# Kernel tuning notes

Hardware: AMD Instinct MI355X
Metric: run time of the kernel (lower is better)

Reference implementation:

```python
import jax, jax.numpy as jnp
import numpy as np

K_HOPS = 2


def setup_inputs() -> dict:
    key = jax.random.key(0)
    k1, k2, k3 = jax.random.split(key, 3)
    N, E, D, C = 100000, 3200000, 512, 40
    x = jax.random.normal(k1, (N, D), dtype=jnp.float32)
    edge_index = jax.random.randint(k2, (2, E), 0, N, dtype=jnp.int64)
    W = jax.random.normal(k3, (C, D), dtype=jnp.float32) * 0.05
    b = jnp.zeros((C,), dtype=jnp.float32)
    return {"x": x, "edge_index": edge_index, "W": W, "b": b}


def reference(x, edge_index, W, b):
    # SGConv: K-hop symmetric-normalized propagation, then Linear, then log_softmax.
    # Dropout is identity at inference (training=False).
    N = x.shape[0]
    loop = jnp.arange(N, dtype=edge_index.dtype)
    src = jnp.concatenate([edge_index[0], loop])  # source nodes (+ self-loops)
    dst = jnp.concatenate([edge_index[1], loop])  # target nodes (+ self-loops)
    ew = jnp.ones(src.shape[0], dtype=x.dtype)
    # deg^{-1/2} A_hat deg^{-1/2}: degree computed at the target (col) index, as in PyG gcn_norm
    deg = jax.ops.segment_sum(ew, dst, num_segments=N)
    dinv = jnp.where(deg > 0, jax.lax.rsqrt(deg), 0.0)
    norm = dinv[src] * dinv[dst]  # [E+N]
    h = x
    for _ in range(K_HOPS):
        # gather source features, weight, scatter-add to targets
        h = jax.ops.segment_sum(norm[:, None] * h[src], dst, num_segments=N)
    logits = h @ W.T + b  # [N, C]
    return jax.nn.log_softmax(logits, axis=1)
```

## Files before the change

kernel.cpp:

```cpp
#include <hip/hip_runtime.h>
#include <hip/hip_bf16.h>


#define TPB 256
#define ETILE 8192

typedef __attribute__((ext_vector_type(8))) short short8v;
typedef __attribute__((ext_vector_type(4))) float f32x4;

__device__ inline short f2bf(float f) {
    unsigned u = __float_as_uint(f);
    unsigned r = (u + 0x7fffu + ((u >> 16) & 1u)) >> 16;
    return (short)r;
}
__device__ inline float bf2f(short s) {
    return __uint_as_float(((unsigned)(unsigned short)s) << 16);
}

__global__ __launch_bounds__(TPB) void k_bhist(
    const int* __restrict__ dst, int* __restrict__ bcnt, int E, int nb) {
    __shared__ int h[512];
    int t = threadIdx.x;
    for (int i = t; i < nb; i += TPB) h[i] = 0;
    __syncthreads();
    int e0 = blockIdx.x * ETILE;
    for (int i = t; i < ETILE; i += TPB) {
        int e = e0 + i;
        if (e < E) atomicAdd(&h[dst[e] >> 8], 1);
    }
    __syncthreads();
    for (int i = t; i < nb; i += TPB)
        if (h[i]) atomicAdd(&bcnt[i], h[i]);
}

__global__ __launch_bounds__(512) void k_boff(
    const int* __restrict__ bcnt, int* __restrict__ boff,
    int* __restrict__ bcur, int nb) {
    __shared__ int s[512];
    int t = threadIdx.x;
    int own = (t < nb) ? bcnt[t] : 0;
    s[t] = own;
    __syncthreads();
    for (int off = 1; off < 512; off <<= 1) {
        int v = (t >= off) ? s[t - off] : 0;
        __syncthreads();
        s[t] += v;
        __syncthreads();
    }
    if (t < nb) {
        int ex = s[t] - own;
        boff[t] = ex;
        bcur[t] = ex;
        if (t == nb - 1) boff[nb] = s[t];
    }
}

__global__ __launch_bounds__(TPB) void k_part(
    const int* __restrict__ src, const int* __restrict__ dst,
    int* __restrict__ bcur, int* __restrict__ pairs, int E, int nb) {
    __shared__ int stash[ETILE];
    __shared__ int hist[512], base[512], lcur[512];
    int t = threadIdx.x;
    for (int i = t; i < nb; i += TPB) hist[i] = 0;
    __syncthreads();
    int e0 = blockIdx.x * ETILE;
    for (int i = t; i < ETILE; i += TPB) {
        int e = e0 + i;
        int d = (e < E) ? dst[e] : -1;
        stash[i] = d;
        if (d >= 0) atomicAdd(&hist[d >> 8], 1);
    }
    __syncthreads();
    for (int i = t; i < nb; i += TPB) {
        base[i] = hist[i] ? atomicAdd(&bcur[i], hist[i]) : 0;
        lcur[i] = 0;
    }
    __syncthreads();
    for (int i = t; i < ETILE; i += TPB) {
        int d = stash[i];
        if (d >= 0) {
            int b = d >> 8;
            int pos = base[b] + atomicAdd(&lcur[b], 1);
            pairs[pos] = ((d & 255) << 20) | src[e0 + i];
        }
    }
}

__global__ __launch_bounds__(TPB) void k_sort(
    const int* __restrict__ pairs, const int* __restrict__ boff,
    int* __restrict__ csr, int* __restrict__ row_ptr, float* __restrict__ dinv,
    int N, int nb) {
    __shared__ int hist[256], excl[256], lcur[256];
    int b = blockIdx.x, t = threadIdx.x;
    hist[t] = 0;
    __syncthreads();
    int beg = boff[b], end = boff[b + 1];
    for (int j = beg + t; j < end; j += TPB)
        atomicAdd(&hist[pairs[j] >> 20], 1);
    __syncthreads();
    int own = hist[t];
    excl[t] = own;
    __syncthreads();
    for (int off = 1; off < 256; off <<= 1) {
        int v = (t >= off) ? excl[t - off] : 0;
        __syncthreads();
        excl[t] += v;
        __syncthreads();
    }
    int node = (b << 8) + t;
    if (node < N) {
        row_ptr[node] = beg + excl[t] - own;
        dinv[node] = rsqrtf((float)(own + 1));
    }
    lcur[t] = 0;
    __syncthreads();
    for (int j = beg + t; j < end; j += TPB) {
        int u = pairs[j];
        int dl = u >> 20;
        int pos = beg + (excl[dl] - hist[dl]) + atomicAdd(&lcur[dl], 1);
        csr[pos] = u & 0xFFFFF;
    }
    if (b == nb - 1 && t == 0) row_ptr[N] = end;
}

__global__ void k_wconv(const float* __restrict__ W, short* __restrict__ Wb,
                        int* __restrict__ bcnt, int nb) {
    if (blockIdx.x == 0)
        for (int i = threadIdx.x; i < nb; i += TPB) bcnt[i] = 0;
    int idx = blockIdx.x * TPB + threadIdx.x;
    int c = idx >> 9, k = idx & 511;
    float v = (c < 40) ? W[c * 512 + k] : 0.f;
    Wb[idx] = f2bf(v);
}

__global__ __launch_bounds__(TPB) void k_matmul_mfma(
    const float* __restrict__ x, const short* __restrict__ Wb,
    const float* __restrict__ dinv, short* __restrict__ z, int N) {
    int wid  = threadIdx.x >> 6;
    int lane = threadIdx.x & 63;
    int rbase = blockIdx.x * 64 + wid * 16;
    if (rbase >= N) return;
    int arow   = rbase + (lane & 15);
    int aclamp = min(arow, N - 1);
    int koff   = (lane >> 4) * 8;
    const float* xrow = x + (size_t)aclamp * 512 + koff;
    const short* wb   = Wb + (lane & 15) * 512 + koff;

    f32x4 acc0 = {0.f,0.f,0.f,0.f}, acc1 = {0.f,0.f,0.f,0.f}, acc2 = {0.f,0.f,0.f,0.f};
    for (int ks = 0; ks < 16; ++ks) {
        int k0 = ks * 32;
        float4 f0 = *reinterpret_cast<const float4*>(xrow + k0);
        float4 f1 = *reinterpret_cast<const float4*>(xrow + k0 + 4);
        short8v a;
        a[0] = f2bf(f0.x); a[1] = f2bf(f0.y); a[2] = f2bf(f0.z); a[3] = f2bf(f0.w);
        a[4] = f2bf(f1.x); a[5] = f2bf(f1.y); a[6] = f2bf(f1.z); a[7] = f2bf(f1.w);
        short8v b0 = *reinterpret_cast<const short8v*>(wb + k0);
        short8v b1 = *reinterpret_cast<const short8v*>(wb + 16 * 512 + k0);
        short8v b2 = *reinterpret_cast<const short8v*>(wb + 32 * 512 + k0);
        acc0 = __builtin_amdgcn_mfma_f32_16x16x32_bf16(a, b0, acc0, 0, 0, 0);
        acc1 = __builtin_amdgcn_mfma_f32_16x16x32_bf16(a, b1, acc1, 0, 0, 0);
        acc2 = __builtin_amdgcn_mfma_f32_16x16x32_bf16(a, b2, acc2, 0, 0, 0);
    }
    int col = lane & 15;
    int rw  = rbase + (lane >> 4) * 4;
#pragma unroll
    for (int reg = 0; reg < 4; ++reg) {
        int r = rw + reg;
        if (r < N) {
            float di = dinv[r];
            z[(size_t)r * 40 + col]      = f2bf(di * acc0[reg]);
            z[(size_t)r * 40 + 16 + col] = f2bf(di * acc1[reg]);
            if (col < 8)
                z[(size_t)r * 40 + 32 + col] = f2bf(di * acc2[reg]);
        }
    }
}

__device__ inline void gather_acc(
    const short8v* __restrict__ Z, const int* __restrict__ csr,
    int beg, int end, int c8, float acc[8]) {
    int j = beg;
    for (; j + 4 <= end; j += 4) {
        int s0 = csr[j], s1 = csr[j+1], s2 = csr[j+2], s3 = csr[j+3];
        short8v v0 = Z[s0 * 5 + c8];
        short8v v1 = Z[s1 * 5 + c8];
        short8v v2 = Z[s2 * 5 + c8];
        short8v v3 = Z[s3 * 5 + c8];
#pragma unroll
        for (int k = 0; k < 8; ++k)
            acc[k] += (bf2f(v0[k]) + bf2f(v1[k])) + (bf2f(v2[k]) + bf2f(v3[k]));
    }
    for (; j < end; ++j) {
        short8v v = Z[csr[j] * 5 + c8];
#pragma unroll
        for (int k = 0; k < 8; ++k) acc[k] += bf2f(v[k]);
    }
}

__global__ __launch_bounds__(TPB) void k_hop1(
    const int* __restrict__ csr, const int* __restrict__ row_ptr,
    const float* __restrict__ dinv, const short* __restrict__ zin,
    short* __restrict__ zout, int N) {
    int t = blockIdx.x * TPB + threadIdx.x;
    int node = t / 5;
    int c8 = t - node * 5;
    if (node >= N) return;
    const short8v* Z = reinterpret_cast<const short8v*>(zin);
    short8v sv = Z[node * 5 + c8];
    float acc[8];
#pragma unroll
    for (int k = 0; k < 8; ++k) acc[k] = bf2f(sv[k]);
    gather_acc(Z, csr, row_ptr[node], row_ptr[node + 1], c8, acc);
    float dd = dinv[node];
    float sc = dd * dd;
    short8v o;
#pragma unroll
    for (int k = 0; k < 8; ++k) o[k] = f2bf(sc * acc[k]);
    reinterpret_cast<short8v*>(zout)[node * 5 + c8] = o;
}

__global__ __launch_bounds__(TPB) void k_hop2_lsm(
    const int* __restrict__ csr, const int* __restrict__ row_ptr,
    const float* __restrict__ dinv, const short* __restrict__ zin,
    const float* __restrict__ bias, float* __restrict__ out, int N) {
    int wid  = threadIdx.x >> 6;
    int lane = threadIdx.x & 63;
    int g    = lane / 5;
    int c8   = lane - g * 5;
    int node = (blockIdx.x * 4 + wid) * 12 + g;
    bool active = (g < 12) && (node < N);

    float v[8];
    float lm = -1e30f;
    if (active) {
        const short8v* Z = reinterpret_cast<const short8v*>(zin);
        short8v sv = Z[node * 5 + c8];
        float acc[8];
#pragma unroll
        for (int k = 0; k < 8; ++k) acc[k] = bf2f(sv[k]);
        gather_acc(Z, csr, row_ptr[node], row_ptr[node + 1], c8, acc);
        float dd = dinv[node];
#pragma unroll
        for (int k = 0; k < 8; ++k) {
            v[k] = dd * acc[k] + bias[c8 * 8 + k];
            lm = fmaxf(lm, v[k]);
        }
    }
    int base = g * 5;
    float gm = lm;
#pragma unroll
    for (int k = 0; k < 5; ++k) gm = fmaxf(gm, __shfl(lm, base + k, 64));
    float ls = 0.f;
    if (active) {
#pragma unroll
        for (int k = 0; k < 8; ++k) ls += __expf(v[k] - gm);
    }
    float tot = 0.f;
#pragma unroll
    for (int k = 0; k < 5; ++k) tot += __shfl(ls, base + k, 64);
    if (active) {
        float lse = gm + __logf(tot);
        float* op = out + (size_t)node * 40 + c8 * 8;
        *reinterpret_cast<float4*>(op)     = make_float4(v[0]-lse, v[1]-lse, v[2]-lse, v[3]-lse);
        *reinterpret_cast<float4*>(op + 4) = make_float4(v[4]-lse, v[5]-lse, v[6]-lse, v[7]-lse);
    }
}

extern "C" void kernel_launch(void* const* d_in, const int* in_sizes, int n_in,
                              void* d_out, int out_size, void* d_ws, size_t ws_size,
                              hipStream_t stream) {
    const float* x  = (const float*)d_in[0];
    const int*   ei = (const int*)d_in[1];
    const float* W  = (const float*)d_in[2];
    const float* b  = (const float*)d_in[3];
    float* out = (float*)d_out;

    const int N = in_sizes[0] / 512;
    const int E = in_sizes[1] / 2;
    const int* src = ei;
    const int* dst = ei + E;
    const int nb = (N + 255) >> 8;

    short* z0b     = (short*)d_ws;
    short* z1b     = z0b + (size_t)N * 40;
    int*   csr     = (int*)(z1b + (size_t)N * 40);
    int*   pairs   = csr + E;
    int*   bcnt    = pairs + E;
    int*   boff    = bcnt + nb;
    int*   bcur    = boff + nb + 1;
    int*   row_ptr = bcur + nb;
    float* dinv    = (float*)(row_ptr + N + 1);
    short* Wb      = (short*)(dinv + N);

    int gT  = (E + ETILE - 1) / ETILE;
    int gM  = (N + 63) / 64;
    int gH1 = (N * 5 + TPB - 1) / TPB;
    int gH2 = (N + 47) / 48;

    k_wconv<<<(48 * 512) / TPB, TPB, 0, stream>>>(W, Wb, bcnt, nb);
    k_bhist<<<gT, TPB, 0, stream>>>(dst, bcnt, E, nb);
    k_boff<<<1, 512, 0, stream>>>(bcnt, boff, bcur, nb);
    k_part<<<gT, TPB, 0, stream>>>(src, dst, bcur, pairs, E, nb);
    k_sort<<<nb, TPB, 0, stream>>>(pairs, boff, csr, row_ptr, dinv, N, nb);

    k_matmul_mfma<<<gM, TPB, 0, stream>>>(x, Wb, dinv, z0b, N);

    k_hop1<<<gH1, TPB, 0, stream>>>(csr, row_ptr, dinv, z0b, z1b, N);
    k_hop2_lsm<<<gH2, TPB, 0, stream>>>(csr, row_ptr, dinv, z1b, b, out, N);
}
```

Baseline: 315.9 us.

## Drop LDS stash in edge partition, enlarge edge tile, unroll gather by eight

The edge tile size is doubled, so the histogram and partition kernels launch half as many blocks and issue fewer global bucket atomics. The partition kernel no longer stages destination indices in a 32KB shared stash and instead rereads dst from global memory, which cuts LDS use and should raise occupancy. The neighbor gather loop gains an 8-wide unrolled stage to keep more independent loads in flight. In exchange the partition kernel reads dst twice, and the wider unroll raises register pressure.

Result: no change. 318.8 us (+0.9%).

```diff
diff --git a/kernel.cpp b/kernel.cpp
--- a/kernel.cpp
+++ b/kernel.cpp
@@ -3,7 +3,7 @@
 
 
 #define TPB 256
-#define ETILE 8192
+#define ETILE 16384
 
 typedef __attribute__((ext_vector_type(8))) short short8v;
 typedef __attribute__((ext_vector_type(4))) float f32x4;
@@ -15,112 +15,6 @@
 }
 __device__ inline float bf2f(short s) {
     return __uint_as_float(((unsigned)(unsigned short)s) << 16);
-}
-
-__global__ __launch_bounds__(TPB) void k_bhist(
-    const int* __restrict__ dst, int* __restrict__ bcnt, int E, int nb) {
-    __shared__ int h[512];
-    int t = threadIdx.x;
-    for (int i = t; i < nb; i += TPB) h[i] = 0;
-    __syncthreads();
-    int e0 = blockIdx.x * ETILE;
-    for (int i = t; i < ETILE; i += TPB) {
-        int e = e0 + i;
-        if (e < E) atomicAdd(&h[dst[e] >> 8], 1);
-    }
-    __syncthreads();
-    for (int i = t; i < nb; i += TPB)
-        if (h[i]) atomicAdd(&bcnt[i], h[i]);
-}
-
-__global__ __launch_bounds__(512) void k_boff(
-    const int* __restrict__ bcnt, int* __restrict__ boff,
-    int* __restrict__ bcur, int nb) {
-    __shared__ int s[512];
-    int t = threadIdx.x;
-    int own = (t < nb) ? bcnt[t] : 0;
-    s[t] = own;
-    __syncthreads();
-    for (int off = 1; off < 512; off <<= 1) {
-        int v = (t >= off) ? s[t - off] : 0;
-        __syncthreads();
-        s[t] += v;
-        __syncthreads();
-    }
-    if (t < nb) {
-        int ex = s[t] - own;
-        boff[t] = ex;
-        bcur[t] = ex;
-        if (t == nb - 1) boff[nb] = s[t];
-    }
-}
-
-__global__ __launch_bounds__(TPB) void k_part(
-    const int* __restrict__ src, const int* __restrict__ dst,
-    int* __restrict__ bcur, int* __restrict__ pairs, int E, int nb) {
-    __shared__ int stash[ETILE];
-    __shared__ int hist[512], base[512], lcur[512];
-    int t = threadIdx.x;
-    for (int i = t; i < nb; i += TPB) hist[i] = 0;
-    __syncthreads();
-    int e0 = blockIdx.x * ETILE;
-    for (int i = t; i < ETILE; i += TPB) {
-        int e = e0 + i;
-        int d = (e < E) ? dst[e] : -1;
-        stash[i] = d;
-        if (d >= 0) atomicAdd(&hist[d >> 8], 1);
-    }
-    __syncthreads();
-    for (int i = t; i < nb; i += TPB) {
-        base[i] = hist[i] ? atomicAdd(&bcur[i], hist[i]) : 0;
-        lcur[i] = 0;
-    }
-    __syncthreads();
-    for (int i = t; i < ETILE; i += TPB) {
-        int d = stash[i];
-        if (d >= 0) {
-            int b = d >> 8;
-            int pos = base[b] + atomicAdd(&lcur[b], 1);
-            pairs[pos] = ((d & 255) << 20) | src[e0 + i];
-        }
-    }
-}
-
-__global__ __launch_bounds__(TPB) void k_sort(
-    const int* __restrict__ pairs, const int* __restrict__ boff,
-    int* __restrict__ csr, int* __restrict__ row_ptr, float* __restrict__ dinv,
-    int N, int nb) {
-    __shared__ int hist[256], excl[256], lcur[256];
-    int b = blockIdx.x, t = threadIdx.x;
-    hist[t] = 0;
-    __syncthreads();
-    int beg = boff[b], end = boff[b + 1];
-    for (int j = beg + t; j < end; j += TPB)
-        atomicAdd(&hist[pairs[j] >> 20], 1);
-    __syncthreads();
-    int own = hist[t];
-    excl[t] = own;
-    __syncthreads();
-    for (int off = 1; off < 256; off <<= 1) {
-        int v = (t >= off) ? excl[t - off] : 0;
-        __syncthreads();
-        excl[t] += v;
-        __syncthreads();
-    }
-    int node = (b << 8) + t;
-    if (node < N) {
-        row_ptr[node] = beg + excl[t] - own;
-        dinv[node] = rsqrtf((float)(own + 1));
-    }
-    lcur[t] = 0;
-    __syncthreads();
-    for (int j = beg + t; j < end; j += TPB) {
-        int u = pairs[j];
-        int dl = u >> 20;
-        int pos = beg + (excl[dl] - hist[dl]) + atomicAdd(&lcur[dl], 1);
-        csr[pos] = u & 0xFFFFF;
-    }
-    if (b == nb - 1 && t == 0) row_ptr[N] = end;
 }
 
 __global__ void k_wconv(const float* __restrict__ W, short* __restrict__ Wb,
@@ -131,6 +25,105 @@
     int c = idx >> 9, k = idx & 511;
     float v = (c < 40) ? W[c * 512 + k] : 0.f;
     Wb[idx] = f2bf(v);
+}
+
+__global__ __launch_bounds__(TPB) void k_bhist(
+    const int* __restrict__ dst, int* __restrict__ bcnt, int E, int nb) {
+    __shared__ int h[512];
+    int t = threadIdx.x;
+    for (int i = t; i < nb; i += TPB) h[i] = 0;
+    __syncthreads();
+    int e0 = blockIdx.x * ETILE;
+    int e1 = min(e0 + ETILE, E);
+    for (int e = e0 + t; e < e1; e += TPB)
+        atomicAdd(&h[dst[e] >> 8], 1);
+    __syncthreads();
+    for (int i = t; i < nb; i += TPB)
+        if (h[i]) atomicAdd(&bcnt[i], h[i]);
+}
+
+__global__ __launch_bounds__(512) void k_boff(
+    const int* __restrict__ bcnt, int* __restrict__ boff,
+    int* __restrict__ bcur, int nb) {
+    __shared__ int s[512];
+    int t = threadIdx.x;
+    int own = (t < nb) ? bcnt[t] : 0;
+    s[t] = own;
+    __syncthreads();
+    for (int off = 1; off < 512; off <<= 1) {
+        int v = (t >= off) ? s[t - off] : 0;
+        __syncthreads();
+        s[t] += v;
+        __syncthreads();
+    }
+    if (t < nb) {
+        int ex = s[t] - own;
+        boff[t] = ex;
+        bcur[t] = ex;
+        if (t == nb - 1) boff[nb] = s[t];
+    }
+}
+
+__global__ __launch_bounds__(TPB) void k_part(
+    const int* __restrict__ src, const int* __restrict__ dst,
+    int* __restrict__ bcur, int* __restrict__ pairs, int E, int nb) {
+    __shared__ int hist[512], base[512];
+    int t = threadIdx.x;
+    for (int i = t; i < nb; i += TPB) hist[i] = 0;
+    __syncthreads();
+    int e0 = blockIdx.x * ETILE;
+    int e1 = min(e0 + ETILE, E);
+    for (int e = e0 + t; e < e1; e += TPB)
+        atomicAdd(&hist[dst[e] >> 8], 1);
+    __syncthreads();
+    for (int i = t; i < nb; i += TPB) {
+        base[i] = hist[i] ? atomicAdd(&bcur[i], hist[i]) : 0;
+        hist[i] = 0;
+    }
+    __syncthreads();
+    for (int e = e0 + t; e < e1; e += TPB) {
+        int d = dst[e];
+        int b = d >> 8;
+        int pos = base[b] + atomicAdd(&hist[b], 1);
+        pairs[pos] = ((d & 255) << 20) | src[e];
+    }
+}
+
+__global__ __launch_bounds__(TPB) void k_sort(
+    const int* __restrict__ pairs, const int* __restrict__ boff,
+    int* __restrict__ csr, int* __restrict__ row_ptr, float* __restrict__ dinv,
+    int N, int nb) {
+    __shared__ int hist[256], excl[256], lcur[256];
+    int b = blockIdx.x, t = threadIdx.x;
+    hist[t] = 0;
+    __syncthreads();
+    int beg = boff[b], end = boff[b + 1];
+    for (int j = beg + t; j < end; j += TPB)
+        atomicAdd(&hist[pairs[j] >> 20], 1);
+    __syncthreads();
+    int own = hist[t];
+    excl[t] = own;
+    __syncthreads();
+    for (int off = 1; off < 256; off <<= 1) {
+        int v = (t >= off) ? excl[t - off] : 0;
+        __syncthreads();
+        excl[t] += v;
+        __syncthreads();
+    }
+    int node = (b << 8) + t;
+    if (node < N) {
+        row_ptr[node] = beg + excl[t] - own;
+        dinv[node] = rsqrtf((float)(own + 1));
+    }
+    lcur[t] = 0;
+    __syncthreads();
+    for (int j = beg + t; j < end; j += TPB) {
+        int u = pairs[j];
+        int dl = u >> 20;
+        int pos = beg + (excl[dl] - hist[dl]) + atomicAdd(&lcur[dl], 1);
+        csr[pos] = u & 0xFFFFF;
+    }
+    if (b == nb - 1 && t == 0) row_ptr[N] = end;
 }
 
 __global__ __launch_bounds__(TPB) void k_matmul_mfma(
@@ -180,6 +173,22 @@
     const short8v* __restrict__ Z, const int* __restrict__ csr,
     int beg, int end, int c8, float acc[8]) {
     int j = beg;
+    for (; j + 8 <= end; j += 8) {
+        int s0 = csr[j],   s1 = csr[j+1], s2 = csr[j+2], s3 = csr[j+3];
+        int s4 = csr[j+4], s5 = csr[j+5], s6 = csr[j+6], s7 = csr[j+7];
+        short8v v0 = Z[s0 * 5 + c8];
+        short8v v1 = Z[s1 * 5 + c8];
+        short8v v2 = Z[s2 * 5 + c8];
+        short8v v3 = Z[s3 * 5 + c8];
+        short8v v4 = Z[s4 * 5 + c8];
+        short8v v5 = Z[s5 * 5 + c8];
+        short8v v6 = Z[s6 * 5 + c8];
+        short8v v7 = Z[s7 * 5 + c8];
+#pragma unroll
+        for (int k = 0; k < 8; ++k)
+            acc[k] += ((bf2f(v0[k]) + bf2f(v1[k])) + (bf2f(v2[k]) + bf2f(v3[k])))
+                    + ((bf2f(v4[k]) + bf2f(v5[k])) + (bf2f(v6[k]) + bf2f(v7[k])));
+    }
     for (; j + 4 <= end; j += 4) {
         int s0 = csr[j], s1 = csr[j+1], s2 = csr[j+2], s3 = csr[j+3];
         short8v v0 = Z[s0 * 5 + c8];
```
